# Kernel optimization log

Hardware: AMD Instinct MI355X
Metric: run time of the kernel (lower is better)

The kernel has to match this reference:

```python
import jax, jax.numpy as jnp
import numpy as np

N = 50000      # nodes
E = 800000     # edges (avg degree 16)
H = 128        # hidden_channels
L = 4          # num_layers
MAXZ = 100
EPS = 1e-5


def setup_inputs() -> dict:
    key = jax.random.key(0)
    ks = jax.random.split(key, 16)
    s = 0.05
    return {
        "z": jax.random.randint(ks[0], (N,), 0, MAXZ),
        "pos": jax.random.normal(ks[1], (N, 3), dtype=jnp.float32),
        "edge_index": jax.random.randint(ks[2], (2, E), 0, N),
        "emb": jax.random.normal(ks[3], (MAXZ, H), dtype=jnp.float32) * s,
        # edge_mlp: Linear(2H+1 -> H), SiLU, Linear(H -> H), SiLU
        "edge_w1": jax.random.normal(ks[4], (L, 2 * H + 1, H), dtype=jnp.float32) * s,
        "edge_b1": jnp.zeros((L, H), dtype=jnp.float32),
        "edge_w2": jax.random.normal(ks[5], (L, H, H), dtype=jnp.float32) * s,
        "edge_b2": jnp.zeros((L, H), dtype=jnp.float32),
        # node_mlp: Linear(2H -> H), SiLU, Linear(H -> H)
        "node_w1": jax.random.normal(ks[6], (L, 2 * H, H), dtype=jnp.float32) * s,
        "node_b1": jnp.zeros((L, H), dtype=jnp.float32),
        "node_w2": jax.random.normal(ks[7], (L, H, H), dtype=jnp.float32) * s,
        "node_b2": jnp.zeros((L, H), dtype=jnp.float32),
        "ln_g": jnp.ones((L, H), dtype=jnp.float32),
        "ln_b": jnp.zeros((L, H), dtype=jnp.float32),
    }


def _layernorm(x, g, b):
    mu = jnp.mean(x, axis=-1, keepdims=True)
    var = jnp.mean((x - mu) ** 2, axis=-1, keepdims=True)
    return g * (x - mu) / jnp.sqrt(var + EPS) + b


def reference(z, pos, edge_index, emb, edge_w1, edge_b1, edge_w2, edge_b2,
              node_w1, node_b1, node_w2, node_b2, ln_g, ln_b):
    row, col = edge_index[0], edge_index[1]
    # update_coords=False: pos is loop-invariant, so rel_pos/dist_sq computed once
    rel = pos[row] - pos[col]                       # [E, 3]
    d2 = jnp.sum(rel * rel, axis=-1, keepdims=True)  # [E, 1]
    h = emb[z]                                       # [N, H]
    n = h.shape[0]
    for l in range(L):
        edge_in = jnp.concatenate([h[row], h[col], d2], axis=-1)  # [E, 2H+1]
        m = jax.nn.silu(edge_in @ edge_w1[l] + edge_b1[l])
        m = jax.nn.silu(m @ edge_w2[l] + edge_b2[l])              # [E, H]
        agg = jax.ops.segment_sum(m, row, num_segments=n)         # [N, H]
        node_in = jnp.concatenate([h, agg], axis=-1)              # [N, 2H]
        h_new = jax.nn.silu(node_in @ node_w1[l] + node_b1[l]) @ node_w2[l] + node_b2[l]
        h = _layernorm(h + h_new, ln_g[l], ln_b[l])
    return h
```

## Files before the change

kernel.cpp:

```cpp
#include <hip/hip_runtime.h>
#include <hip/hip_bf16.h>

typedef __hip_bfloat16 hipbf16;

#define H 128
#define NLAYERS 4
#define LN_EPS 1e-5f
#define ET 64

typedef __bf16 bf16x8 __attribute__((ext_vector_type(8)));
typedef unsigned short ushort8 __attribute__((ext_vector_type(8)));
typedef float floatx16 __attribute__((ext_vector_type(16)));

union frag_u { ushort8 u; bf16x8 b; };

__device__ __forceinline__ float silu(float x) {
    return x * __builtin_amdgcn_rcpf(1.f + __expf(-x));
}
__device__ __forceinline__ float b2f_bits(unsigned short u) { return __uint_as_float(((unsigned)u) << 16); }
__device__ __forceinline__ unsigned short f2b(float f) {
    unsigned u = __float_as_uint(f);
    unsigned r = ((u >> 16) & 1u) + 0x7fffu;
    return (unsigned short)((u + r) >> 16);
}

__global__ void detect_kernel(const unsigned short* __restrict__ p, int nHalf,
                              int* __restrict__ flag) {
    int t = threadIdx.x;
    int bad = 0;
    for (int i = t; i < nHalf; i += 64) {
        unsigned short u = p[i];
        int e = (u >> 7) & 0xFF;
        if (e >= 0x8E) bad = 1;
    }
    unsigned long long m = __ballot(bad != 0);
    if (t == 0) *flag = (m != 0ULL) ? 1 : 0;
}

__global__ void conv_kernel(const void* __restrict__ src, float* __restrict__ dst,
                            int n, const int* __restrict__ flag) {
    int i = blockIdx.x * blockDim.x + threadIdx.x;
    if (i >= n) return;
    if (*flag) dst[i] = ((const float*)src)[i];
    else       dst[i] = b2f_bits(((const unsigned short*)src)[i]);
}

__global__ void pack_kernel(const float* __restrict__ W, unsigned short* __restrict__ blob,
                            int ksteps) {
    int idx = blockIdx.x * 256 + threadIdx.x;
    if (idx >= ksteps * 2048) return;
    int j  = idx & 7;
    int L  = (idx >> 3) & 63;
    int nt = (idx >> 9) & 3;
    int ks = idx >> 11;
    int k = ks * 16 + (L >> 5) * 8 + j;
    int n = nt * 32 + (L & 31);
    blob[idx] = f2b(W[k * H + n]);
}

__global__ void embed_kernel(const int* __restrict__ z, const float* __restrict__ emb,
                             float* __restrict__ h, unsigned short* __restrict__ hb, int n) {
    int idx = blockIdx.x * blockDim.x + threadIdx.x;
    if (idx >= n * H) return;
    int i = idx >> 7, j = idx & 127;
    float v = emb[z[i] * H + j];
    h[idx] = v;
    hb[idx] = f2b(v);
}

__global__ void hist_kernel(const int* __restrict__ row, int* __restrict__ cnt, int nE) {
    int i = blockIdx.x * blockDim.x + threadIdx.x;
    if (i < nE) atomicAdd(&cnt[row[i]], 1);
}

__global__ __launch_bounds__(1024) void scan_kernel(const int* __restrict__ cnt,
                                                    int* __restrict__ rptr,
                                                    int* __restrict__ cur, int nN) {
    __shared__ int wsum[17];
    __shared__ int s_carry;
    int t = threadIdx.x;
    if (t == 0) s_carry = 0;
    __syncthreads();
    for (int base = 0; base < nN; base += 1024) {
        int i = base + t;
        int v = (i < nN) ? cnt[i] : 0;
        int x = v;
        #pragma unroll
        for (int off = 1; off < 64; off <<= 1) {
            int y = __shfl_up(x, off);
            if ((t & 63) >= off) x += y;
        }
        if ((t & 63) == 63) wsum[t >> 6] = x;
        __syncthreads();
        if (t == 0) {
            int s = 0;
            #pragma unroll
            for (int w = 0; w < 16; ++w) { int tmp = wsum[w]; wsum[w] = s; s += tmp; }
            wsum[16] = s;
        }
        __syncthreads();
        int cin = s_carry;
        int excl = cin + wsum[t >> 6] + (x - v);
        if (i < nN) { rptr[i] = excl; cur[i] = excl; }
        __syncthreads();
        if (t == 0) s_carry = cin + wsum[16];
        __syncthreads();
    }
    if (t == 0) rptr[nN] = s_carry;
}

__global__ void scatter_kernel(const int* __restrict__ row, const int* __restrict__ col,
                               const float* __restrict__ pos,
                               int* __restrict__ cur,
                               int* __restrict__ rowsS, int* __restrict__ colsS,
                               float* __restrict__ d2S, int nE) {
    int e = blockIdx.x * blockDim.x + threadIdx.x;
    if (e >= nE) return;
    int r = row[e], c = col[e];
    int p = atomicAdd(&cur[r], 1);
    rowsS[p] = r;
    colsS[p] = c;
    float dx = pos[r * 3 + 0] - pos[c * 3 + 0];
    float dy = pos[r * 3 + 1] - pos[c * 3 + 1];
    float dz = pos[r * 3 + 2] - pos[c * 3 + 2];
    d2S[p] = dx * dx + dy * dy + dz * dz;
}

__global__ __launch_bounds__(256, 2) void edge_hyb(
    const unsigned short* __restrict__ hb,
    const int* __restrict__ rowsS, const int* __restrict__ colsS,
    const float* __restrict__ d2S,
    const unsigned short* __restrict__ pb1, const float* __restrict__ b1,
    const float* __restrict__ w1last,
    const unsigned short* __restrict__ pb2, const float* __restrict__ b2,
    float* __restrict__ agg, int nE)
{
    __shared__ __align__(16) unsigned short sT[ET * 136];

    const int t = threadIdx.x;
    const int wv = t >> 6, lane = t & 63;
    const int wm = wv & 1, wn = wv >> 1;
    const int lm = lane & 31, lh = lane >> 5;
    const int n0 = wn * 64 + lm;
    const int p0 = blockIdx.x * ET;

    const int p = p0 + wm * 32 + lm;
    const bool valid = p < nE;
    const int pc = valid ? p : (nE - 1);
    const int nrow = rowsS[pc];
    const int ncol = colsS[pc];
    const float dd = d2S[pc];
    const int ptag = valid ? nrow : -1;

    const unsigned short* rowp = hb + (size_t)nrow * H + lh * 8;
    const unsigned short* colp = hb + (size_t)ncol * H + lh * 8;

    const float bias10 = b1[n0], bias11 = b1[n0 + 32];
    const float wl0 = w1last[n0], wl1 = w1last[n0 + 32];
    const float bias20 = b2[n0], bias21 = b2[n0 + 32];

    floatx16 acc0 = {}, acc1 = {};
    #pragma unroll
    for (int ks = 0; ks < 16; ++ks) {
        frag_u a, fb0, fb1;
        a.u = (ks < 8) ? *(const ushort8*)(rowp + ks * 16)
                       : *(const ushort8*)(colp + (ks - 8) * 16);
        fb0.u = *(const ushort8*)(pb1 + (size_t)((ks * 4 + wn * 2 + 0) * 64 + lane) * 8);
        fb1.u = *(const ushort8*)(pb1 + (size_t)((ks * 4 + wn * 2 + 1) * 64 + lane) * 8);
        acc0 = __builtin_amdgcn_mfma_f32_32x32x16_bf16(a.b, fb0.b, acc0, 0, 0, 0);
        acc1 = __builtin_amdgcn_mfma_f32_32x32x16_bf16(a.b, fb1.b, acc1, 0, 0, 0);
    }

    #pragma unroll
    for (int r = 0; r < 16; ++r) {
        int mi = (r & 3) + 8 * (r >> 2) + 4 * lh;
        int m = wm * 32 + mi;
        float dm = __shfl(dd, mi);
        sT[m * 136 + n0]      = f2b(silu(acc0[r] + bias10 + dm * wl0));
        sT[m * 136 + n0 + 32] = f2b(silu(acc1[r] + bias11 + dm * wl1));
    }
    __syncthreads();

    floatx16 c0 = {}, c1 = {};
    const unsigned short* A2 = sT + (wm * 32 + lm) * 136 + lh * 8;
    #pragma unroll
    for (int ks = 0; ks < 8; ++ks) {
        frag_u a, fb0, fb1;
        a.u   = *(const ushort8*)(A2 + ks * 16);
        fb0.u = *(const ushort8*)(pb2 + (size_t)((ks * 4 + wn * 2 + 0) * 64 + lane) * 8);
        fb1.u = *(const ushort8*)(pb2 + (size_t)((ks * 4 + wn * 2 + 1) * 64 + lane) * 8);
        c0 = __builtin_amdgcn_mfma_f32_32x32x16_bf16(a.b, fb0.b, c0, 0, 0, 0);
        c1 = __builtin_amdgcn_mfma_f32_32x32x16_bf16(a.b, fb1.b, c1, 0, 0, 0);
    }

    #pragma unroll
    for (int g = 0; g < 4; ++g) {
        const int mi0 = 4 * lh + 8 * g;
        int prow = __shfl(ptag, mi0);
        float s0 = silu(c0[g * 4] + bias20);
        float s1 = silu(c1[g * 4] + bias21);
        #pragma unroll
        for (int k = 1; k < 4; ++k) {
            int rw = __shfl(ptag, mi0 + k);
            float u0 = silu(c0[g * 4 + k] + bias20);
            float u1 = silu(c1[g * 4 + k] + bias21);
            if (rw == prow) {
                s0 += u0; s1 += u1;
            } else {
                if (prow >= 0) {
                    atomicAdd(&agg[(size_t)prow * H + n0],      s0);
                    atomicAdd(&agg[(size_t)prow * H + n0 + 32], s1);
                }
                prow = rw; s0 = u0; s1 = u1;
            }
        }
        if (prow >= 0) {
            atomicAdd(&agg[(size_t)prow * H + n0],      s0);
            atomicAdd(&agg[(size_t)prow * H + n0 + 32], s1);
        }
    }
}

__global__ __launch_bounds__(256) void node_mfma(
    const unsigned short* __restrict__ hb,
    const float* __restrict__ aggf,
    const unsigned short* __restrict__ pn1, const float* __restrict__ b1,
    const unsigned short* __restrict__ pn2, const float* __restrict__ b2,
    float* __restrict__ hnew, int nN)
{
    __shared__ __align__(16) unsigned short sA[ET * 264];

    const int t = threadIdx.x;
    const int i0 = blockIdx.x * ET;

    #pragma unroll
    for (int c = t; c < ET * 32; c += 256) {
        int e = c >> 5;
        int node = i0 + e; if (node >= nN) node = nN - 1;
        int f0 = (c & 31) * 8;
        ushort8 v;
        if (f0 < H) {
            v = *(const ushort8*)(hb + (size_t)node * H + f0);
        } else {
            const float* src = aggf + (size_t)node * H + (f0 - H);
            #pragma unroll
            for (int j = 0; j < 8; ++j) v[j] = f2b(src[j]);
        }
        *(ushort8*)(sA + e * 264 + (c & 31) * 8) = v;
    }
    __syncthreads();

    const int lane = t & 63;
    const int wv = t >> 6;
    const int wm = wv & 1, wn = wv >> 1;
    const int lm = lane & 31, lh = lane >> 5;
    const int n0 = wn * 64 + lm;

    floatx16 acc0 = {}, acc1 = {};
    const unsigned short* A0 = sA + (wm * 32 + lm) * 264 + lh * 8;
    #pragma unroll
    for (int ks = 0; ks < 16; ++ks) {
        frag_u a, fb0, fb1;
        a.u   = *(const ushort8*)(A0 + ks * 16);
        fb0.u = *(const ushort8*)(pn1 + (size_t)((ks * 4 + wn * 2 + 0) * 64 + lane) * 8);
        fb1.u = *(const ushort8*)(pn1 + (size_t)((ks * 4 + wn * 2 + 1) * 64 + lane) * 8);
        acc0 = __builtin_amdgcn_mfma_f32_32x32x16_bf16(a.b, fb0.b, acc0, 0, 0, 0);
        acc1 = __builtin_amdgcn_mfma_f32_32x32x16_bf16(a.b, fb1.b, acc1, 0, 0, 0);
    }
    __syncthreads();

    unsigned short* sT = sA;
    {
        float bias0 = b1[n0], bias1 = b1[n0 + 32];
        #pragma unroll
        for (int r = 0; r < 16; ++r) {
            int m = wm * 32 + (r & 3) + 8 * (r >> 2) + 4 * lh;
            sT[m * 136 + n0]      = f2b(silu(acc0[r] + bias0));
            sT[m * 136 + n0 + 32] = f2b(silu(acc1[r] + bias1));
        }
    }
    __syncthreads();

    floatx16 c0 = {}, c1 = {};
    const unsigned short* A2 = sT + (wm * 32 + lm) * 136 + lh * 8;
    #pragma unroll
    for (int ks = 0; ks < 8; ++ks) {
        frag_u a, fb0, fb1;
        a.u   = *(const ushort8*)(A2 + ks * 16);
        fb0.u = *(const ushort8*)(pn2 + (size_t)((ks * 4 + wn * 2 + 0) * 64 + lane) * 8);
        fb1.u = *(const ushort8*)(pn2 + (size_t)((ks * 4 + wn * 2 + 1) * 64 + lane) * 8);
        c0 = __builtin_amdgcn_mfma_f32_32x32x16_bf16(a.b, fb0.b, c0, 0, 0, 0);
        c1 = __builtin_amdgcn_mfma_f32_32x32x16_bf16(a.b, fb1.b, c1, 0, 0, 0);
    }
    {
        float bias0 = b2[n0], bias1 = b2[n0 + 32];
        #pragma unroll
        for (int r = 0; r < 16; ++r) {
            int m = wm * 32 + (r & 3) + 8 * (r >> 2) + 4 * lh;
            int node = i0 + m;
            if (node < nN) {
                float* dst = hnew + (size_t)node * H;
                dst[n0]      = c0[r] + bias0;
                dst[n0 + 32] = c1[r] + bias1;
            }
        }
    }
}

__global__ __launch_bounds__(256) void ln_kernel(
    float* __restrict__ h, unsigned short* __restrict__ hb,
    const float* __restrict__ hnew,
    const float* __restrict__ G, const float* __restrict__ B, int nN)
{
    __shared__ float rs[4], rq[4];
    int t = threadIdx.x;
    int local = t >> 7, j = t & 127;
    int i = blockIdx.x * 2 + local;
    float v = 0.f;
    if (i < nN) v = h[(size_t)i * H + j] + hnew[(size_t)i * H + j];
    float s = v, q = v * v;
    #pragma unroll
    for (int off = 32; off > 0; off >>= 1) {
        s += __shfl_down(s, off);
        q += __shfl_down(q, off);
    }
    int w = t >> 6;
    if ((t & 63) == 0) { rs[w] = s; rq[w] = q; }
    __syncthreads();
    int w0 = local * 2;
    float S = rs[w0] + rs[w0 + 1], Q = rq[w0] + rq[w0 + 1];
    float mu = S * (1.f / H);
    float var = Q * (1.f / H) - mu * mu;
    float y = (v - mu) * rsqrtf(var + LN_EPS) * G[j] + B[j];
    if (i < nN) {
        h[(size_t)i * H + j] = y;
        hb[(size_t)i * H + j] = f2b(y);
    }
}

__global__ void cast_kernel(const float* __restrict__ h, void* __restrict__ out,
                            int n, const int* __restrict__ flag) {
    int idx = blockIdx.x * blockDim.x + threadIdx.x;
    if (idx >= n) return;
    if (*flag) ((float*)out)[idx] = h[idx];
    else       ((hipbf16*)out)[idx] = __float2bfloat16(h[idx]);
}

extern "C" void kernel_launch(void* const* d_in, const int* in_sizes, int n_in,
                              void* d_out, int out_size, void* d_ws, size_t ws_size,
                              hipStream_t stream)
{
    const int* z  = (const int*)d_in[0];
    const int* ei = (const int*)d_in[2];

    const int nN = in_sizes[0];
    const int nE = in_sizes[2] / 2;
    const int* row = ei;
    const int* col = ei + nE;

    float* ws   = (float*)d_ws;
    int*   flag = (int*)ws;
    float* h    = ws + 64;
    unsigned short* hb = (unsigned short*)(h + (size_t)nN * H);
    float* agg  = (float*)(hb + (size_t)nN * H);
    float* conv = agg + (size_t)nN * H;

    const int n_pos = in_sizes[1];
    const int n_emb = in_sizes[3];
    const int n_ew1 = in_sizes[4], n_eb1 = in_sizes[5];
    const int n_ew2 = in_sizes[6], n_eb2 = in_sizes[7];
    const int n_nw1 = in_sizes[8], n_nb1 = in_sizes[9];
    const int n_nw2 = in_sizes[10], n_nb2 = in_sizes[11];
    const int n_lng = in_sizes[12], n_lnb = in_sizes[13];

    float* pos = conv;
    float* emb = pos + n_pos;
    float* ew1 = emb + n_emb;
    float* eb1 = ew1 + n_ew1;
    float* ew2 = eb1 + n_eb1;
    float* eb2 = ew2 + n_ew2;
    float* nw1 = eb2 + n_eb2;
    float* nb1 = nw1 + n_nw1;
    float* nw2 = nb1 + n_nb1;
    float* nb2 = nw2 + n_nw2;
    float* lng = nb2 + n_nb2;
    float* lnb = lng + n_lng;
    float* conv_end = lnb + n_lnb;

    unsigned short* pb1 = (unsigned short*)conv_end;
    unsigned short* pb2 = pb1 + 4 * 32768;
    unsigned short* pn1 = pb2 + 4 * 16384;
    unsigned short* pn2 = pn1 + 4 * 32768;

    int* cnt   = (int*)(pn2 + 4 * 16384);
    int* rptr  = cnt + nN;
    int* cur   = rptr + nN + 1;
    int* rowsS = cur + nN;
    int* colsS = rowsS + nE;
    float* d2S = (float*)(colsS + nE);

    detect_kernel<<<1, 64, 0, stream>>>((const unsigned short*)d_in[4], 4096, flag);

    struct { const void* src; float* dst; int n; } cv[12] = {
        {d_in[1],  pos, n_pos}, {d_in[3],  emb, n_emb},
        {d_in[4],  ew1, n_ew1}, {d_in[5],  eb1, n_eb1},
        {d_in[6],  ew2, n_ew2}, {d_in[7],  eb2, n_eb2},
        {d_in[8],  nw1, n_nw1}, {d_in[9],  nb1, n_nb1},
        {d_in[10], nw2, n_nw2}, {d_in[11], nb2, n_nb2},
        {d_in[12], lng, n_lng}, {d_in[13], lnb, n_lnb},
    };
    for (int i = 0; i < 12; ++i)
        conv_kernel<<<(cv[i].n + 255) / 256, 256, 0, stream>>>(cv[i].src, cv[i].dst, cv[i].n, flag);

    for (int l = 0; l < NLAYERS; ++l) {
        pack_kernel<<<128, 256, 0, stream>>>(ew1 + (size_t)l * 257 * H, pb1 + l * 32768, 16);
        pack_kernel<<<64,  256, 0, stream>>>(ew2 + (size_t)l * H * H,   pb2 + l * 16384, 8);
        pack_kernel<<<128, 256, 0, stream>>>(nw1 + (size_t)l * 2 * H * H, pn1 + l * 32768, 16);
        pack_kernel<<<64,  256, 0, stream>>>(nw2 + (size_t)l * H * H,   pn2 + l * 16384, 8);
    }

    hipMemsetAsync(cnt, 0, (size_t)nN * sizeof(int), stream);
    hist_kernel<<<(nE + 255) / 256, 256, 0, stream>>>(row, cnt, nE);
    scan_kernel<<<1, 1024, 0, stream>>>(cnt, rptr, cur, nN);
    scatter_kernel<<<(nE + 255) / 256, 256, 0, stream>>>(row, col, pos, cur, rowsS, colsS, d2S, nE);

    embed_kernel<<<(nN * H + 255) / 256, 256, 0, stream>>>(z, emb, h, hb, nN);

    const int nTiles = (nE + ET - 1) / ET;
    const int nTilesN = (nN + ET - 1) / ET;
    for (int l = 0; l < NLAYERS; ++l) {
        hipMemsetAsync(agg, 0, (size_t)nN * H * sizeof(float), stream);
        edge_hyb<<<nTiles, 256, 0, stream>>>(
            hb, rowsS, colsS, d2S,
            pb1 + l * 32768, eb1 + (size_t)l * H,
            ew1 + (size_t)l * 257 * H + 256 * H,
            pb2 + l * 16384, eb2 + (size_t)l * H,
            agg, nE);
        node_mfma<<<nTilesN, 256, 0, stream>>>(
            hb, agg,
            pn1 + l * 32768, nb1 + (size_t)l * H,
            pn2 + l * 16384, nb2 + (size_t)l * H,
            agg , nN);
        ln_kernel<<<(nN + 1) / 2, 256, 0, stream>>>(
            h, hb, agg, lng + (size_t)l * H, lnb + (size_t)l * H, nN);
    }
    cast_kernel<<<(nN * H + 255) / 256, 256, 0, stream>>>(h, d_out, nN * H, flag);
}
```

Baseline: 1.520 ms.

## Double edge tile to 128 rows per block to reuse weight fragments

```diff
diff --git a/kernel.cpp b/kernel.cpp
--- a/kernel.cpp
+++ b/kernel.cpp
@@ -7,6 +7,7 @@
 #define NLAYERS 4
 #define LN_EPS 1e-5f
 #define ET 64
+#define EB 128
 
 typedef __bf16 bf16x8 __attribute__((ext_vector_type(8)));
 typedef unsigned short ushort8 __attribute__((ext_vector_type(8)));
@@ -126,7 +127,7 @@
     d2S[p] = dx * dx + dy * dy + dz * dz;
 }
 
-__global__ __launch_bounds__(256, 2) void edge_hyb(
+__global__ __launch_bounds__(256, 2) void edge_big(
     const unsigned short* __restrict__ hb,
     const int* __restrict__ rowsS, const int* __restrict__ colsS,
     const float* __restrict__ d2S,
@@ -135,88 +136,110 @@
     const unsigned short* __restrict__ pb2, const float* __restrict__ b2,
     float* __restrict__ agg, int nE)
 {
-    __shared__ __align__(16) unsigned short sT[ET * 136];
+    __shared__ __align__(16) unsigned short sT[EB * 136];
 
     const int t = threadIdx.x;
     const int wv = t >> 6, lane = t & 63;
     const int wm = wv & 1, wn = wv >> 1;
     const int lm = lane & 31, lh = lane >> 5;
     const int n0 = wn * 64 + lm;
-    const int p0 = blockIdx.x * ET;
-
-    const int p = p0 + wm * 32 + lm;
-    const bool valid = p < nE;
-    const int pc = valid ? p : (nE - 1);
-    const int nrow = rowsS[pc];
-    const int ncol = colsS[pc];
-    const float dd = d2S[pc];
-    const int ptag = valid ? nrow : -1;
-
-    const unsigned short* rowp = hb + (size_t)nrow * H + lh * 8;
-    const unsigned short* colp = hb + (size_t)ncol * H + lh * 8;
+    const int p0 = blockIdx.x * EB;
+
+    int ptag[2]; float dd[2];
+    const unsigned short *rowp[2], *colp[2];
+    #pragma unroll
+    for (int s = 0; s < 2; ++s) {
+        int p = p0 + wm * 64 + s * 32 + lm;
+        bool valid = p < nE;
+        int pc = valid ? p : (nE - 1);
+        int nr = rowsS[pc], nc = colsS[pc];
+        dd[s] = d2S[pc];
+        ptag[s] = valid ? nr : -1;
+        rowp[s] = hb + (size_t)nr * H + lh * 8;
+        colp[s] = hb + (size_t)nc * H + lh * 8;
+    }
 
     const float bias10 = b1[n0], bias11 = b1[n0 + 32];
     const float wl0 = w1last[n0], wl1 = w1last[n0 + 32];
     const float bias20 = b2[n0], bias21 = b2[n0 + 32];
 
-    floatx16 acc0 = {}, acc1 = {};
+    floatx16 a00 = {}, a01 = {}, a10 = {}, a11 = {};
     #pragma unroll
     for (int ks = 0; ks < 16; ++ks) {
-        frag_u a, fb0, fb1;
-        a.u = (ks < 8) ? *(const ushort8*)(rowp + ks * 16)
-                       : *(const ushort8*)(colp + (ks - 8) * 16);
+        frag_u fb0, fb1;
         fb0.u = *(const ushort8*)(pb1 + (size_t)((ks * 4 + wn * 2 + 0) * 64 + lane) * 8);
         fb1.u = *(const ushort8*)(pb1 + (size_t)((ks * 4 + wn * 2 + 1) * 64 + lane) * 8);
-        acc0 = __builtin_amdgcn_mfma_f32_32x32x16_bf16(a.b, fb0.b, acc0, 0, 0, 0);
-        acc1 = __builtin_amdgcn_mfma_f32_32x32x16_bf16(a.b, fb1.b, acc1, 0, 0, 0);
-    }
-
-    #pragma unroll
-    for (int r = 0; r < 16; ++r) {
-        int mi = (r & 3) + 8 * (r >> 2) + 4 * lh;
-        int m = wm * 32 + mi;
-        float dm = __shfl(dd, mi);
-        sT[m * 136 + n0]      = f2b(silu(acc0[r] + bias10 + dm * wl0));
-        sT[m * 136 + n0 + 32] = f2b(silu(acc1[r] + bias11 + dm * wl1));
-    }
-    __syncthreads();
-
-    floatx16 c0 = {}, c1 = {};
-    const unsigned short* A2 = sT + (wm * 32 + lm) * 136 + lh * 8;
+        frag_u x0, x1;
+        x0.u = (ks < 8) ? *(const ushort8*)(rowp[0] + ks * 16)
+                        : *(const ushort8*)(colp[0] + (ks - 8) * 16);
+        x1.u = (ks < 8) ? *(const ushort8*)(rowp[1] + ks * 16)
+                        : *(const ushort8*)(colp[1] + (ks - 8) * 16);
+        a00 = __builtin_amdgcn_mfma_f32_32x32x16_bf16(x0.b, fb0.b, a00, 0, 0, 0);
+        a01 = __builtin_amdgcn_mfma_f32_32x32x16_bf16(x0.b, fb1.b, a01, 0, 0, 0);
+        a10 = __builtin_amdgcn_mfma_f32_32x32x16_bf16(x1.b, fb0.b, a10, 0, 0, 0);
+        a11 = __builtin_amdgcn_mfma_f32_32x32x16_bf16(x1.b, fb1.b, a11, 0, 0, 0);
+    }
+
+    #pragma unroll
+    for (int s = 0; s < 2; ++s) {
+        const floatx16& u0 = s ? a10 : a00;
+        const floatx16& u1 = s ? a11 : a01;
+        #pragma unroll
+        for (int r = 0; r < 16; ++r) {
+            int mi = (r & 3) + 8 * (r >> 2) + 4 * lh;
+            int m = wm * 64 + s * 32 + mi;
+            float dm = __shfl(dd[s], mi);
+            sT[m * 136 + n0]      = f2b(silu(u0[r] + bias10 + dm * wl0));
+            sT[m * 136 + n0 + 32] = f2b(silu(u1[r] + bias11 + dm * wl1));
+        }
+    }
+    __syncthreads();
+
+    floatx16 c00 = {}, c01 = {}, c10 = {}, c11 = {};
+    const unsigned short* A20 = sT + (wm * 64 + lm) * 136 + lh * 8;
+    const unsigned short* A21 = sT + (wm * 64 + 32 + lm) * 136 + lh * 8;
     #pragma unroll
     for (int ks = 0; ks < 8; ++ks) {
-        frag_u a, fb0, fb1;
-        a.u   = *(const ushort8*)(A2 + ks * 16);
+        frag_u fb0, fb1, x0, x1;
         fb0.u = *(const ushort8*)(pb2 + (size_t)((ks * 4 + wn * 2 + 0) * 64 + lane) * 8);
         fb1.u = *(const ushort8*)(pb2 + (size_t)((ks * 4 + wn * 2 + 1) * 64 + lane) * 8);
-        c0 = __builtin_amdgcn_mfma_f32_32x32x16_bf16(a.b, fb0.b, c0, 0, 0, 0);
-        c1 = __builtin_amdgcn_mfma_f32_32x32x16_bf16(a.b, fb1.b, c1, 0, 0, 0);
-    }
-
-    #pragma unroll
-    for (int g = 0; g < 4; ++g) {
-        const int mi0 = 4 * lh + 8 * g;
-        int prow = __shfl(ptag, mi0);
-        float s0 = silu(c0[g * 4] + bias20);
-        float s1 = silu(c1[g * 4] + bias21);
+        x0.u = *(const ushort8*)(A20 + ks * 16);
+        x1.u = *(const ushort8*)(A21 + ks * 16);
+        c00 = __builtin_amdgcn_mfma_f32_32x32x16_bf16(x0.b, fb0.b, c00, 0, 0, 0);
+        c01 = __builtin_amdgcn_mfma_f32_32x32x16_bf16(x0.b, fb1.b, c01, 0, 0, 0);
+        c10 = __builtin_amdgcn_mfma_f32_32x32x16_bf16(x1.b, fb0.b, c10, 0, 0, 0);
+        c11 = __builtin_amdgcn_mfma_f32_32x32x16_bf16(x1.b, fb1.b, c11, 0, 0, 0);
+    }
+
+    #pragma unroll
+    for (int s = 0; s < 2; ++s) {
+        const floatx16& u0 = s ? c10 : c00;
+        const floatx16& u1 = s ? c11 : c01;
         #pragma unroll
-        for (int k = 1; k < 4; ++k) {
-            int rw = __shfl(ptag, mi0 + k);
-            float u0 = silu(c0[g * 4 + k] + bias20);
-            float u1 = silu(c1[g * 4 + k] + bias21);
-            if (rw == prow) {
-                s0 += u0; s1 += u1;
-            } else {
-                if (prow >= 0) {
-                    atomicAdd(&agg[(size_t)prow * H + n0],      s0);
-                    atomicAdd(&agg[(size_t)prow * H + n0 + 32], s1);
+        for (int g = 0; g < 4; ++g) {
+            const int mi0 = 4 * lh + 8 * g;
+            int prow = __shfl(ptag[s], mi0);
+            float s0 = silu(u0[g * 4] + bias20);
+            float s1 = silu(u1[g * 4] + bias21);
+            #pragma unroll
+            for (int k = 1; k < 4; ++k) {
+                int rw = __shfl(ptag[s], mi0 + k);
+                float v0 = silu(u0[g * 4 + k] + bias20);
+                float v1 = silu(u1[g * 4 + k] + bias21);
+                if (rw == prow) {
+                    s0 += v0; s1 += v1;
+                } else {
+                    if (prow >= 0) {
+                        atomicAdd(&agg[(size_t)prow * H + n0],      s0);
+                        atomicAdd(&agg[(size_t)prow * H + n0 + 32], s1);
+                    }
+                    prow = rw; s0 = v0; s1 = v1;
                 }
-                prow = rw; s0 = u0; s1 = u1;
             }
-        }
-        if (prow >= 0) {
-            atomicAdd(&agg[(size_t)prow * H + n0],      s0);
-            atomicAdd(&agg[(size_t)prow * H + n0 + 32], s1);
+            if (prow >= 0) {
+                atomicAdd(&agg[(size_t)prow * H + n0],      s0);
+                atomicAdd(&agg[(size_t)prow * H + n0 + 32], s1);
+            }
         }
     }
 }
@@ -426,11 +449,11 @@
 
     embed_kernel<<<(nN * H + 255) / 256, 256, 0, stream>>>(z, emb, h, hb, nN);
 
-    const int nTiles = (nE + ET - 1) / ET;
+    const int nTilesE = (nE + EB - 1) / EB;
     const int nTilesN = (nN + ET - 1) / ET;
     for (int l = 0; l < NLAYERS; ++l) {
         hipMemsetAsync(agg, 0, (size_t)nN * H * sizeof(float), stream);
-        edge_hyb<<<nTiles, 256, 0, stream>>>(
+        edge_big<<<nTilesE, 256, 0, stream>>>(
             hb, rowsS, colsS, d2S,
             pb1 + l * 32768, eb1 + (size_t)l * H,
             ew1 + (size_t)l * 257 * H + 256 * H,
```

Measured after the change: 1.601 ms. +5.3%, slower.

## Precompute per-node first-layer projections and gather them per edge

Applied to the files above, without the earlier changes.

```diff
diff --git a/kernel.cpp b/kernel.cpp
--- a/kernel.cpp
+++ b/kernel.cpp
@@ -58,14 +58,25 @@
     blob[idx] = f2b(W[k * H + n]);
 }
 
+__global__ void pack_cat(const float* __restrict__ W1, unsigned short* __restrict__ blob) {
+    int idx = blockIdx.x * 256 + threadIdx.x;
+    if (idx >= 32768) return;
+    int j  = idx & 7;
+    int L  = (idx >> 3) & 63;
+    int nt = (idx >> 9) & 7;
+    int ks = idx >> 12;
+    int k = ks * 16 + (L >> 5) * 8 + j;
+    int f = nt * 32 + (L & 31);
+    float v = (f < H) ? W1[k * H + f] : W1[(H + k) * H + (f - H)];
+    blob[idx] = f2b(v);
+}
+
 __global__ void embed_kernel(const int* __restrict__ z, const float* __restrict__ emb,
-                             float* __restrict__ h, unsigned short* __restrict__ hb, int n) {
+                             unsigned short* __restrict__ hb, int n) {
     int idx = blockIdx.x * blockDim.x + threadIdx.x;
     if (idx >= n * H) return;
     int i = idx >> 7, j = idx & 127;
-    float v = emb[z[i] * H + j];
-    h[idx] = v;
-    hb[idx] = f2b(v);
+    hb[idx] = f2b(emb[z[i] * H + j]);
 }
 
 __global__ void hist_kernel(const int* __restrict__ row, int* __restrict__ cnt, int nE) {
@@ -126,17 +137,50 @@
     d2S[p] = dx * dx + dy * dy + dz * dz;
 }
 
-__global__ __launch_bounds__(256, 2) void edge_hyb(
+__global__ __launch_bounds__(256) void proj_kernel(
     const unsigned short* __restrict__ hb,
+    const unsigned short* __restrict__ pcat, const float* __restrict__ b1,
+    unsigned short* __restrict__ P, int nN)
+{
+    const int t = threadIdx.x;
+    const int wv = t >> 6, lane = t & 63;
+    const int lm = lane & 31, lh = lane >> 5;
+    const int i0 = blockIdx.x * 32;
+    const int node = min(i0 + lm, nN - 1);
+    const unsigned short* ap = hb + (size_t)node * H + lh * 8;
+    const int n0 = wv * 64 + lm;
+
+    floatx16 c0 = {}, c1 = {};
+    #pragma unroll
+    for (int ks = 0; ks < 8; ++ks) {
+        frag_u a, fb0, fb1;
+        a.u   = *(const ushort8*)(ap + ks * 16);
+        fb0.u = *(const ushort8*)(pcat + (size_t)((ks * 8 + wv * 2 + 0) * 64 + lane) * 8);
+        fb1.u = *(const ushort8*)(pcat + (size_t)((ks * 8 + wv * 2 + 1) * 64 + lane) * 8);
+        c0 = __builtin_amdgcn_mfma_f32_32x32x16_bf16(a.b, fb0.b, c0, 0, 0, 0);
+        c1 = __builtin_amdgcn_mfma_f32_32x32x16_bf16(a.b, fb1.b, c1, 0, 0, 0);
+    }
+    const float bias0 = (n0 < H)      ? b1[n0]      : 0.f;
+    const float bias1 = (n0 + 32 < H) ? b1[n0 + 32] : 0.f;
+    #pragma unroll
+    for (int r = 0; r < 16; ++r) {
+        int m = (r & 3) + 8 * (r >> 2) + 4 * lh;
+        int nd = i0 + m;
+        if (nd < nN) {
+            P[(size_t)nd * 256 + n0]      = f2b(c0[r] + bias0);
+            P[(size_t)nd * 256 + n0 + 32] = f2b(c1[r] + bias1);
+        }
+    }
+}
+
+__global__ __launch_bounds__(256) void edge_p(
+    const unsigned short* __restrict__ P,
     const int* __restrict__ rowsS, const int* __restrict__ colsS,
     const float* __restrict__ d2S,
-    const unsigned short* __restrict__ pb1, const float* __restrict__ b1,
     const float* __restrict__ w1last,
-    const unsigned short* __restrict__ pb2, const float* __restrict__ b2,
+    const unsigned short* __restrict__ pb2, const float* __restrict__ b2v,
     float* __restrict__ agg, int nE)
 {
-    __shared__ __align__(16) unsigned short sT[ET * 136];
-
     const int t = threadIdx.x;
     const int wv = t >> 6, lane = t & 63;
     const int wm = wv & 1, wn = wv >> 1;
@@ -152,43 +196,28 @@
     const float dd = d2S[pc];
     const int ptag = valid ? nrow : -1;
 
-    const unsigned short* rowp = hb + (size_t)nrow * H + lh * 8;
-    const unsigned short* colp = hb + (size_t)ncol * H + lh * 8;
-
-    const float bias10 = b1[n0], bias11 = b1[n0 + 32];
-    const float wl0 = w1last[n0], wl1 = w1last[n0 + 32];
-    const float bias20 = b2[n0], bias21 = b2[n0 + 32];
-
-    floatx16 acc0 = {}, acc1 = {};
-    #pragma unroll
-    for (int ks = 0; ks < 16; ++ks) {
-        frag_u a, fb0, fb1;
-        a.u = (ks < 8) ? *(const ushort8*)(rowp + ks * 16)
-                       : *(const ushort8*)(colp + (ks - 8) * 16);
-        fb0.u = *(const ushort8*)(pb1 + (size_t)((ks * 4 + wn * 2 + 0) * 64 + lane) * 8);
-        fb1.u = *(const ushort8*)(pb1 + (size_t)((ks * 4 + wn * 2 + 1) * 64 + lane) * 8);
-        acc0 = __builtin_amdgcn_mfma_f32_32x32x16_bf16(a.b, fb0.b, acc0, 0, 0, 0);
-        acc1 = __builtin_amdgcn_mfma_f32_32x32x16_bf16(a.b, fb1.b, acc1, 0, 0, 0);
-    }
-
-    #pragma unroll
-    for (int r = 0; r < 16; ++r) {
-        int mi = (r & 3) + 8 * (r >> 2) + 4 * lh;
-        int m = wm * 32 + mi;
-        float dm = __shfl(dd, mi);
-        sT[m * 136 + n0]      = f2b(silu(acc0[r] + bias10 + dm * wl0));
-        sT[m * 136 + n0 + 32] = f2b(silu(acc1[r] + bias11 + dm * wl1));
-    }
-    __syncthreads();
+    const unsigned short* pap = P + (size_t)nrow * 256 + lh * 8;
+    const unsigned short* pbp = P + (size_t)ncol * 256 + 128 + lh * 8;
+    const float* wlp = w1last + lh * 8;
+
+    const float bias20 = b2v[n0], bias21 = b2v[n0 + 32];
 
     floatx16 c0 = {}, c1 = {};
-    const unsigned short* A2 = sT + (wm * 32 + lm) * 136 + lh * 8;
     #pragma unroll
     for (int ks = 0; ks < 8; ++ks) {
-        frag_u a, fb0, fb1;
-        a.u   = *(const ushort8*)(A2 + ks * 16);
+        frag_u pa, pb, a, fb0, fb1;
+        pa.u  = *(const ushort8*)(pap + ks * 16);
+        pb.u  = *(const ushort8*)(pbp + ks * 16);
         fb0.u = *(const ushort8*)(pb2 + (size_t)((ks * 4 + wn * 2 + 0) * 64 + lane) * 8);
         fb1.u = *(const ushort8*)(pb2 + (size_t)((ks * 4 + wn * 2 + 1) * 64 + lane) * 8);
+        float4 wl0 = *(const float4*)(wlp + ks * 16);
+        float4 wl1 = *(const float4*)(wlp + ks * 16 + 4);
+        float wls[8] = {wl0.x, wl0.y, wl0.z, wl0.w, wl1.x, wl1.y, wl1.z, wl1.w};
+        #pragma unroll
+        for (int j = 0; j < 8; ++j) {
+            float v = b2f_bits(pa.u[j]) + b2f_bits(pb.u[j]) + dd * wls[j];
+            a.u[j] = f2b(silu(v));
+        }
         c0 = __builtin_amdgcn_mfma_f32_32x32x16_bf16(a.b, fb0.b, c0, 0, 0, 0);
         c1 = __builtin_amdgcn_mfma_f32_32x32x16_bf16(a.b, fb1.b, c1, 0, 0, 0);
     }
@@ -308,7 +337,7 @@
 }
 
 __global__ __launch_bounds__(256) void ln_kernel(
-    float* __restrict__ h, unsigned short* __restrict__ hb,
+    unsigned short* __restrict__ hb,
     const float* __restrict__ hnew,
     const float* __restrict__ G, const float* __restrict__ B, int nN)
 {
@@ -317,7 +346,7 @@
     int local = t >> 7, j = t & 127;
     int i = blockIdx.x * 2 + local;
     float v = 0.f;
-    if (i < nN) v = h[(size_t)i * H + j] + hnew[(size_t)i * H + j];
+    if (i < nN) v = b2f_bits(hb[(size_t)i * H + j]) + hnew[(size_t)i * H + j];
     float s = v, q = v * v;
     #pragma unroll
     for (int off = 32; off > 0; off >>= 1) {
@@ -332,18 +361,15 @@
     float mu = S * (1.f / H);
     float var = Q * (1.f / H) - mu * mu;
     float y = (v - mu) * rsqrtf(var + LN_EPS) * G[j] + B[j];
-    if (i < nN) {
-        h[(size_t)i * H + j] = y;
-        hb[(size_t)i * H + j] = f2b(y);
-    }
-}
-
-__global__ void cast_kernel(const float* __restrict__ h, void* __restrict__ out,
+    if (i < nN) hb[(size_t)i * H + j] = f2b(y);
+}
+
+__global__ void cast_kernel(const unsigned short* __restrict__ hb, void* __restrict__ out,
                             int n, const int* __restrict__ flag) {
     int idx = blockIdx.x * blockDim.x + threadIdx.x;
     if (idx >= n) return;
-    if (*flag) ((float*)out)[idx] = h[idx];
-    else       ((hipbf16*)out)[idx] = __float2bfloat16(h[idx]);
+    if (*flag) ((float*)out)[idx] = b2f_bits(hb[idx]);
+    else       ((unsigned short*)out)[idx] = hb[idx];
 }
 
 extern "C" void kernel_launch(void* const* d_in, const int* in_sizes, int n_in,
@@ -360,10 +386,10 @@
 
     float* ws   = (float*)d_ws;
     int*   flag = (int*)ws;
-    float* h    = ws + 64;
-    unsigned short* hb = (unsigned short*)(h + (size_t)nN * H);
+    unsigned short* hb = (unsigned short*)(ws + 64);
     float* agg  = (float*)(hb + (size_t)nN * H);
-    float* conv = agg + (size_t)nN * H;
+    unsigned short* P = (unsigned short*)(agg + (size_t)nN * H);
+    float* conv = (float*)(P + (size_t)nN * 256);
 
     const int n_pos = in_sizes[1];
     const int n_emb = in_sizes[3];
@@ -387,12 +413,12 @@
     float* lnb = lng + n_lng;
     float* conv_end = lnb + n_lnb;
 
-    unsigned short* pb1 = (unsigned short*)conv_end;
-    unsigned short* pb2 = pb1 + 4 * 32768;
-    unsigned short* pn1 = pb2 + 4 * 16384;
-    unsigned short* pn2 = pn1 + 4 * 32768;
-
-    int* cnt   = (int*)(pn2 + 4 * 16384);
+    unsigned short* pb2  = (unsigned short*)conv_end;
+    unsigned short* pn1  = pb2 + 4 * 16384;
+    unsigned short* pn2  = pn1 + 4 * 32768;
+    unsigned short* pcat = pn2 + 4 * 16384;
+
+    int* cnt   = (int*)(pcat + 4 * 32768);
     int* rptr  = cnt + nN;
     int* cur   = rptr + nN + 1;
     int* rowsS = cur + nN;
@@ -413,7 +439,7 @@
         conv_kernel<<<(cv[i].n + 255) / 256, 256, 0, stream>>>(cv[i].src, cv[i].dst, cv[i].n, flag);
 
     for (int l = 0; l < NLAYERS; ++l) {
-        pack_kernel<<<128, 256, 0, stream>>>(ew1 + (size_t)l * 257 * H, pb1 + l * 32768, 16);
+        pack_cat<<<128, 256, 0, stream>>>(ew1 + (size_t)l * 257 * H, pcat + l * 32768);
         pack_kernel<<<64,  256, 0, stream>>>(ew2 + (size_t)l * H * H,   pb2 + l * 16384, 8);
         pack_kernel<<<128, 256, 0, stream>>>(nw1 + (size_t)l * 2 * H * H, pn1 + l * 32768, 16);
         pack_kernel<<<64,  256, 0, stream>>>(nw2 + (size_t)l * H * H,   pn2 + l * 16384, 8);
@@ -424,15 +450,17 @@
     scan_kernel<<<1, 1024, 0, stream>>>(cnt, rptr, cur, nN);
     scatter_kernel<<<(nE + 255) / 256, 256, 0, stream>>>(row, col, pos, cur, rowsS, colsS, d2S, nE);
 
-    embed_kernel<<<(nN * H + 255) / 256, 256, 0, stream>>>(z, emb, h, hb, nN);
-
-    const int nTiles = (nE + ET - 1) / ET;
+    embed_kernel<<<(nN * H + 255) / 256, 256, 0, stream>>>(z, emb, hb, nN);
+
+    const int nTilesE = (nE + ET - 1) / ET;
     const int nTilesN = (nN + ET - 1) / ET;
+    const int nTilesP = (nN + 31) / 32;
     for (int l = 0; l < NLAYERS; ++l) {
+        proj_kernel<<<nTilesP, 256, 0, stream>>>(
+            hb, pcat + l * 32768, eb1 + (size_t)l * H, P, nN);
         hipMemsetAsync(agg, 0, (size_t)nN * H * sizeof(float), stream);
-        edge_hyb<<<nTiles, 256, 0, stream>>>(
-            hb, rowsS, colsS, d2S,
-            pb1 + l * 32768, eb1 + (size_t)l * H,
+        edge_p<<<nTilesE, 256, 0, stream>>>(
+            P, rowsS, colsS, d2S,
             ew1 + (size_t)l * 257 * H + 256 * H,
             pb2 + l * 16384, eb2 + (size_t)l * H,
             agg, nE);
@@ -442,7 +470,7 @@
             pn2 + l * 16384, nb2 + (size_t)l * H,
             agg , nN);
         ln_kernel<<<(nN + 1) / 2, 256, 0, stream>>>(
-            h, hb, agg, lng + (size_t)l * H, lnb + (size_t)l * H, nN);
-    }
-    cast_kernel<<<(nN * H + 255) / 256, 256, 0, stream>>>(h, d_out, nN * H, flag);
-}
+            hb, agg, lng + (size_t)l * H, lnb + (size_t)l * H, nN);
+    }
+    cast_kernel<<<(nN * H + 255) / 256, 256, 0, stream>>>(hb, d_out, nN * H, flag);
+}
```

After: 1.481 ms. -2.6%, faster.
